# Kernel tuning notes

Measured on AMD Instinct MI355X. Metric: run time of the kernel, lower is better.

Reference implementation:

```python
import jax, jax.numpy as jnp
import numpy as np

BATCH = 32
NUM_PRIORS = 8732
NUM_CLASSES = 81          # includes background class 0
CENTER_VAR = 0.1
SIZE_VAR = 0.2
CONF_THR = 0.01
NMS_THR = 0.45
TOPK = 100                # per-class NMS candidates
MAX_DET = 100             # max detections per image


def setup_inputs() -> dict:
    key = jax.random.key(0)
    k1, k2, k3 = jax.random.split(key, 3)
    cls_logits = jax.random.normal(k1, (BATCH, NUM_PRIORS, NUM_CLASSES), jnp.float32)
    bbox_pred = jax.random.normal(k2, (BATCH, NUM_PRIORS, 4), jnp.float32)
    # center-form priors (cx, cy, w, h) in (0, 1)
    priors = jax.random.uniform(k3, (NUM_PRIORS, 4), jnp.float32, 0.05, 0.95)
    return {"cls_logits": cls_logits, "bbox_pred": bbox_pred, "priors": priors}


def _decode(loc, priors):
    # convert_locations_to_boxes (center form) then center_form_to_corner_form
    cxcy = loc[..., :2] * CENTER_VAR * priors[..., 2:] + priors[..., :2]
    wh = jnp.exp(loc[..., 2:] * SIZE_VAR) * priors[..., 2:]
    return jnp.concatenate([cxcy - wh * 0.5, cxcy + wh * 0.5], axis=-1)  # [.., 4] xyxy


def _pairwise_iou(b):
    # b: [K, 4] corner form
    lt = jnp.maximum(b[:, None, :2], b[None, :, :2])
    rb = jnp.minimum(b[:, None, 2:], b[None, :, 2:])
    wh = jnp.clip(rb - lt, 0.0)
    inter = wh[..., 0] * wh[..., 1]
    area = jnp.clip(b[:, 2] - b[:, 0], 0.0) * jnp.clip(b[:, 3] - b[:, 1], 0.0)
    return inter / (area[:, None] + area[None, :] - inter + 1e-9)


def _per_class_nms(scores_n, boxes_n):
    # scores_n: [N], boxes_n: [N, 4]
    s, idx = jax.lax.top_k(scores_n, TOPK)
    b = boxes_n[idx]                                # [K, 4]
    iou = _pairwise_iou(b)                          # [K, K]
    init = s > CONF_THR
    rng = jnp.arange(TOPK)

    def body(i, keep):
        sup = (iou[i] > NMS_THR) & keep[i] & (rng > i)
        return keep & ~sup

    keep = jax.lax.fori_loop(0, TOPK, body, init)   # greedy NMS on sorted boxes
    return jnp.where(keep, s, 0.0), b


def reference(cls_logits, bbox_pred, priors):
    scores = jax.nn.softmax(cls_logits, axis=-1)            # [B, N, C]
    boxes = _decode(bbox_pred, priors)                      # [B, N, 4]
    cls_scores = jnp.swapaxes(scores[..., 1:], 1, 2)        # [B, C-1, N] skip background
    nms_fn = jax.vmap(jax.vmap(_per_class_nms, in_axes=(0, None)), in_axes=(0, 0))
    s_k, b_k = nms_fn(cls_scores, boxes)                    # [B, C-1, K], [B, C-1, K, 4]
    labels = jnp.broadcast_to(jnp.arange(1, NUM_CLASSES)[None, :, None], s_k.shape)
    B = s_k.shape[0]
    flat = (NUM_CLASSES - 1) * TOPK
    s_f = s_k.reshape(B, flat)
    b_f = b_k.reshape(B, flat, 4)
    l_f = labels.reshape(B, flat)
    top_s, top_i = jax.lax.top_k(s_f, MAX_DET)              # keep best MAX_DET per image
    top_b = jnp.take_along_axis(b_f, top_i[..., None], axis=1)
    top_l = jnp.take_along_axis(l_f, top_i, axis=1)
    return top_b, top_s, top_l.astype(jnp.int32)
```

## Files before the change

kernel.cpp:

```cpp
#include <hip/hip_runtime.h>
#include <hip/hip_bf16.h>
#include <float.h>

#define BATCH    32
#define NPRIORS  8732
#define NT32     274
#define NPAD     (NT32 * 32)
#define NCLASSES 81
#define NC1      80
#define TOPK     100
#define MAXDET   100
#define FLATC    (NC1 * TOPK)
#define FV4      2000
#define NCAND    512
#define NBIN     1024
#define BINOFF   3040
#define NK4      (NT32 * 4)

__global__ __launch_bounds__(256, 4) void softmax_stats_kernel(
    const float* __restrict__ logits, unsigned short* __restrict__ key16,
    float2* __restrict__ stats) {
  int b = blockIdx.x / NT32;
  int tile = blockIdx.x - b * NT32;
  int n0 = tile * 32;
  int rows = min(32, NPRIORS - n0);

  int t = threadIdx.x;
  int r = t >> 3;
  int q = t & 7;

  __shared__ __align__(16) unsigned int ldsu[NC1 * 16];

  const bool live = (r < rows);

  unsigned int out16[10];
  if (live) {
    const float* rowp = logits + ((size_t)b * NPRIORS + n0 + r) * NCLASSES;
    float v[11];
#pragma unroll
    for (int k = 0; k < 10; ++k) v[k] = rowp[q + (k << 3)];
    v[10] = (q == 0) ? rowp[80] : -FLT_MAX;

    float m = -FLT_MAX;
#pragma unroll
    for (int k = 0; k < 10; ++k) m = fmaxf(m, v[k]);
    if (q == 0) m = fmaxf(m, v[10]);
    m = fmaxf(m, __shfl_xor(m, 1));
    m = fmaxf(m, __shfl_xor(m, 2));
    m = fmaxf(m, __shfl_xor(m, 4));

    float s = 0.f;
#pragma unroll
    for (int k = 0; k < 10; ++k) {
      v[k] = expf(v[k] - m);
      s += v[k];
    }
    if (q == 0) {
      v[10] = expf(v[10] - m);
      s += v[10];
    }
    s += __shfl_xor(s, 1);
    s += __shfl_xor(s, 2);
    s += __shfl_xor(s, 4);

#pragma unroll
    for (int k = 0; k < 10; ++k) {
      float sc = v[k] / s;
      out16[k] = __float_as_uint(sc) >> 16;
    }
    if (q == 0) out16[0] = __float_as_uint(v[10] / s) >> 16;
    if (q == 0) stats[(size_t)b * NPAD + n0 + r] = make_float2(m, s);
  } else {
#pragma unroll
    for (int k = 0; k < 10; ++k) out16[k] = 0u;
  }

#pragma unroll
  for (int k = 0; k < 10; ++k) {
    unsigned int part = (unsigned int)__shfl_xor((int)out16[k], 8);
    if ((r & 1) == 0) {
      int cls = (q == 0) ? ((k == 0) ? 79 : (8 * k - 1)) : (q - 1 + 8 * k);
      ldsu[cls * 16 + (r >> 1)] = out16[k] | (part << 16);
    }
  }
  __syncthreads();

  uint4* dst = (uint4*)(key16 + (size_t)(b * NT32 + tile) * (NC1 * 32));
  for (int i = t; i < 320; i += 256) dst[i] = ((const uint4*)ldsu)[i];
}

__device__ __forceinline__ float4 decode_box(float4 l, float4 p) {
  float cx = l.x * 0.1f * p.z + p.x;
  float cy = l.y * 0.1f * p.w + p.y;
  float w  = expf(l.z * 0.2f) * p.z;
  float h  = expf(l.w * 0.2f) * p.w;
  return make_float4(cx - w * 0.5f, cy - h * 0.5f, cx + w * 0.5f,
                     cy + h * 0.5f);
}

__device__ __forceinline__ unsigned long long cex(unsigned long long key,
                                                  unsigned long long p,
                                                  bool up, bool low) {
  return (up == low) ? (key < p ? key : p) : (key > p ? key : p);
}

__global__ __launch_bounds__(256, 8) void topk_select_kernel(
    const unsigned short* __restrict__ key16,
    const float* __restrict__ logits, const float2* __restrict__ stats,
    unsigned long long* __restrict__ k_sel) {
  const int bc = blockIdx.x;
  const int b = bc / NC1;
  const int c = bc - b * NC1;
  const int t = threadIdx.x;
  const int lane = t & 63;
  const int w = t >> 6;

  __shared__ __align__(16) unsigned int hist[NBIN * 2];
  __shared__ __align__(16) unsigned long long cand[NCAND];
  __shared__ __align__(16) unsigned int cidx[NCAND];
  __shared__ int s_cnt, s_cut, wtot[4];

  const uint4* k4 = (const uint4*)key16;
  const size_t base4 = (size_t)b * (NT32 * NC1 * 4) + (size_t)c * 4;

  uint4 va4[5];
#pragma unroll
  for (int i = 0; i < 5; ++i) {
    int p4 = t + (i << 8);
    uint4 v = make_uint4(0u, 0u, 0u, 0u);
    if (p4 < NK4) v = k4[base4 + (size_t)(p4 >> 2) * (NC1 * 4) + (p4 & 3)];
    va4[i] = v;
  }
#pragma unroll
  for (int i = 0; i < 5; ++i)
    asm volatile("" : "+v"(va4[i].x), "+v"(va4[i].y), "+v"(va4[i].z),
                      "+v"(va4[i].w));

  uint4* h4 = (uint4*)hist;
  const uint4 z4 = make_uint4(0u, 0u, 0u, 0u);
  h4[t] = z4;
  h4[t + 256] = z4;
  if (t == 0) { s_cnt = 0; s_cut = 0; }
  __syncthreads();

#pragma unroll
  for (int i = 0; i < 5; ++i) {
    const unsigned int* cp = (const unsigned int*)&va4[i];
#pragma unroll
    for (int u = 0; u < 4; ++u) {
      unsigned int cc = cp[u];
      unsigned int lo = cc & 0xFFFFu, hi = cc >> 16;
      if (lo) {
        int bin = (int)(lo >> 2) - BINOFF;
        bin = max(0, min(NBIN - 1, bin));
        atomicAdd(&hist[(bin << 1) | (lane & 1)], 1u);
      }
      if (hi) {
        int bin = (int)(hi >> 2) - BINOFF;
        bin = max(0, min(NBIN - 1, bin));
        atomicAdd(&hist[(bin << 1) | (lane & 1)], 1u);
      }
    }
  }
  __syncthreads();

  int h[4];
  int ls;
  {
    uint4 a = h4[2 * t];
    uint4 b2 = h4[2 * t + 1];
    h[0] = (int)(a.x + a.y);
    h[1] = (int)(a.z + a.w);
    h[2] = (int)(b2.x + b2.y);
    h[3] = (int)(b2.z + b2.w);
    ls = h[0] + h[1] + h[2] + h[3];
  }
  int s = ls;
#pragma unroll
  for (int off = 1; off < 64; off <<= 1) {
    int o = __shfl_down(s, off);
    if (lane + off < 64) s += o;
  }
  if (lane == 0) wtot[w] = s;
  __syncthreads();
  int upper = 0;
  for (int w2 = w + 1; w2 < 4; ++w2) upper += wtot[w2];
  int run = (s - ls) + upper;
  int cutbin = -1;
#pragma unroll
  for (int k = 3; k >= 0; --k) {
    if (run < TOPK && run + h[k] >= TOPK) cutbin = (t << 2) + k;
    run += h[k];
  }
  if (cutbin >= 0) s_cut = cutbin;
  __syncthreads();

  const unsigned int cutk = (unsigned int)(s_cut + BINOFF) << 2;

  unsigned long long msk = 0ull;
  int cnt = 0;
#pragma unroll
  for (int i = 0; i < 5; ++i) {
    const unsigned int* cp = (const unsigned int*)&va4[i];
#pragma unroll
    for (int u = 0; u < 4; ++u) {
      unsigned int cc = cp[u];
      if ((cc & 0xFFFFu) >= cutk) { msk |= 1ull << (i * 8 + u * 2); ++cnt; }
      if ((cc >> 16) >= cutk)     { msk |= 1ull << (i * 8 + u * 2 + 1); ++cnt; }
    }
  }
  int inc = cnt;
#pragma unroll
  for (int off = 1; off < 64; off <<= 1) {
    int o = __shfl_up(inc, off);
    if (lane >= off) inc += o;
  }
  int wtotal = __shfl(inc, 63);
  int wbase = 0;
  if (lane == 63) wbase = atomicAdd(&s_cnt, wtotal);
  wbase = __shfl(wbase, 63);
  int pos = wbase + inc - cnt;
#pragma unroll
  for (int i = 0; i < 5; ++i) {
    int p4 = t + (i << 8);
    int bpr = ((p4 >> 2) << 5) + ((p4 & 3) << 3);
#pragma unroll
    for (int j = 0; j < 8; ++j) {
      if ((msk >> (i * 8 + j)) & 1ull) {
        if (pos < NCAND) cidx[pos] = (unsigned int)(bpr + j);
        ++pos;
      }
    }
  }
  __syncthreads();

  const int ncand = min(s_cnt, NCAND);

  unsigned long long key = ~0ull;
  if (t < ncand) {
    int p = (int)cidx[t];
    float l = logits[((size_t)b * NPRIORS + p) * NCLASSES + (c + 1)];
    float2 st = stats[(size_t)b * NPAD + p];
    float sc = expf(l - st.x) / st.y;
    key = (((unsigned long long)(~__float_as_uint(sc))) << 32) |
          (unsigned int)p;
  }

  if (ncand <= 256) {
#pragma unroll
    for (int k2 = 2; k2 <= 256; k2 <<= 1) {
#pragma unroll
      for (int j = 128; j > 0; j >>= 1) {
        if (j >= k2) continue;
        const bool up = ((t & k2) == 0);
        if (j >= 64) {
          cand[t] = key;
          __syncthreads();
          unsigned long long p = cand[t ^ j];
          key = cex(key, p, up, (t & j) == 0);
          __syncthreads();
        } else {
          unsigned long long p = __shfl_xor(key, j);
          key = cex(key, p, up, (lane & j) == 0);
        }
      }
    }
    if (t < TOPK) k_sel[(size_t)bc * TOPK + t] = key;
  } else {
    unsigned long long key2 = ~0ull;
    if (t + 256 < ncand) {
      int p = (int)cidx[t + 256];
      float l = logits[((size_t)b * NPRIORS + p) * NCLASSES + (c + 1)];
      float2 st = stats[(size_t)b * NPAD + p];
      float sc = expf(l - st.x) / st.y;
      key2 = (((unsigned long long)(~__float_as_uint(sc))) << 32) |
             (unsigned int)p;
    }
    cand[t] = key;
    cand[t + 256] = key2;
    __syncthreads();
    int NS = 512;
    for (int k2 = 2; k2 <= NS; k2 <<= 1) {
      for (int j = k2 >> 1; j > 0; j >>= 1) {
        if (j >= 128) {
          __syncthreads();
          for (int p = t; p < NS; p += 256) {
            int ixj = p ^ j;
            if (ixj > p) {
              unsigned long long a = cand[p], c2 = cand[ixj];
              bool up = ((p & k2) == 0);
              if (up ? (a > c2) : (a < c2)) { cand[p] = c2; cand[ixj] = a; }
            }
          }
          __syncthreads();
        } else {
          int base = w << 7;
          if (base < NS) {
#pragma unroll
            for (int half = 0; half < 2; ++half) {
              int p = base + lane + (half << 6);
              int ixj = p ^ j;
              if (ixj > p) {
                unsigned long long a = cand[p], c2 = cand[ixj];
                bool up = ((p & k2) == 0);
                if (up ? (a > c2) : (a < c2)) { cand[p] = c2; cand[ixj] = a; }
              }
            }
          }
        }
      }
    }
    __syncthreads();
    if (t < TOPK) k_sel[(size_t)bc * TOPK + t] = cand[t];
  }
}

__global__ __launch_bounds__(256) void nms_kernel(
    const unsigned long long* __restrict__ k_sel,
    const float* __restrict__ loc, const float* __restrict__ priors,
    float* __restrict__ s_k, float* __restrict__ b_k) {
  const int t = threadIdx.x;
  const int lane = t & 63;
  const int w = t >> 6;
  const int bc = blockIdx.x;
  const int b = bc / NC1;

  __shared__ __align__(16) float4 lbox[TOPK];
  __shared__ float larea[TOPK];
  __shared__ float lscore[TOPK];
  __shared__ unsigned long long pm[4][64][3];
  __shared__ unsigned long long keepw[2];

  if (t < TOPK) {
    unsigned long long key = k_sel[(size_t)bc * TOPK + t];
    float sv = __uint_as_float(~(unsigned int)(key >> 32));
    int idx = (int)(key & 0xFFFFFFFFull);
    if ((unsigned)idx >= NPRIORS) { idx = 0; sv = 0.f; }
    float4 bx = decode_box(((const float4*)loc)[(size_t)b * NPRIORS + idx],
                           ((const float4*)priors)[idx]);
    lbox[t] = bx;
    larea[t] = fmaxf(bx.z - bx.x, 0.f) * fmaxf(bx.w - bx.y, 0.f);
    lscore[t] = sv;
  }
  __syncthreads();

  const bool hasb = (lane + 64) < TOPK;
  float4 ba = lbox[lane];
  float aa = larea[lane];
  float4 bb2 = lbox[hasb ? (lane + 64) : 0];
  float ab = larea[hasb ? (lane + 64) : 0];

  unsigned long long ra0 = 0, ra1 = 0, rb1 = 0;
  int jlo = max(1, w * 25);
  int jhi = min(TOPK, w * 25 + 25);
  for (int j = jlo; j < jhi; ++j) {
    float4 bj = lbox[j];
    float aj = larea[j];
    if (lane < j) {
      float iw = fmaxf(fminf(ba.z, bj.z) - fmaxf(ba.x, bj.x), 0.f);
      float ih = fmaxf(fminf(ba.w, bj.w) - fmaxf(ba.y, bj.y), 0.f);
      float inter = iw * ih;
      float iou = inter / (aa + aj - inter + 1e-9f);
      if (iou > 0.45f) {
        if (j < 64) ra0 |= 1ull << j; else ra1 |= 1ull << (j - 64);
      }
    }
    if (hasb && (lane + 64) < j) {
      float iw = fmaxf(fminf(bb2.z, bj.z) - fmaxf(bb2.x, bj.x), 0.f);
      float ih = fmaxf(fminf(bb2.w, bj.w) - fmaxf(bb2.y, bj.y), 0.f);
      float inter = iw * ih;
      float iou = inter / (ab + aj - inter + 1e-9f);
      if (iou > 0.45f) rb1 |= 1ull << (j - 64);
    }
  }
  pm[w][lane][0] = ra0;
  pm[w][lane][1] = ra1;
  pm[w][lane][2] = rb1;
  __syncthreads();

  if (w == 0) {
    unsigned long long fa0 = pm[0][lane][0] | pm[1][lane][0] |
                             pm[2][lane][0] | pm[3][lane][0];
    unsigned long long fa1 = pm[0][lane][1] | pm[1][lane][1] |
                             pm[2][lane][1] | pm[3][lane][1];
    unsigned long long fb1 = pm[0][lane][2] | pm[1][lane][2] |
                             pm[2][lane][2] | pm[3][lane][2];

    float sva = lscore[lane];
    float svb = hasb ? lscore[lane + 64] : 0.f;
    unsigned long long keep0 = __ballot(sva > 0.01f);
    unsigned long long keep1 = __ballot(hasb && (svb > 0.01f));
    for (int i = 0; i < TOPK; ++i) {
      bool il = i < 64;
      bool kb = il ? ((keep0 >> i) & 1ull) : ((keep1 >> (i - 64)) & 1ull);
      unsigned long long m0 = __shfl(il ? fa0 : 0ull, i & 63);
      unsigned long long m1 = __shfl(il ? fa1 : fb1, i & 63);
      if (kb) { keep0 &= ~m0; keep1 &= ~m1; }
    }
    if (lane == 0) { keepw[0] = keep0; keepw[1] = keep1; }
  }
  __syncthreads();

  if (t < TOPK) {
    bool kp = (t < 64) ? ((keepw[0] >> t) & 1ull)
                       : ((keepw[1] >> (t - 64)) & 1ull);
    s_k[(size_t)bc * TOPK + t] = kp ? lscore[t] : 0.f;
    ((float4*)(b_k + (size_t)bc * TOPK * 4))[t] = lbox[t];
  }
}

__global__ __launch_bounds__(256) void final_topk_kernel(
    const float* __restrict__ s_k, const float* __restrict__ b_k,
    float* __restrict__ out) {
  const int b = blockIdx.x;
  const int t = threadIdx.x;
  const int lane = t & 63;
  const int w = t >> 6;

  __shared__ __align__(16) unsigned int hist[NBIN * 2];
  __shared__ __align__(16) unsigned long long cand[NCAND];
  __shared__ int s_cnt, s_cut, wtot[4];

  const float4* src4 = (const float4*)(s_k + (size_t)b * FLATC);

  float va[32];
#pragma unroll
  for (int i = 0; i < 8; ++i) {
    int p = t + (i << 8);
    float4 v = make_float4(0.f, 0.f, 0.f, 0.f);
    if (p < FV4) v = src4[p];
    va[4 * i + 0] = v.x; va[4 * i + 1] = v.y;
    va[4 * i + 2] = v.z; va[4 * i + 3] = v.w;
  }

  uint4* h4 = (uint4*)hist;
  const uint4 z4 = make_uint4(0u, 0u, 0u, 0u);
  h4[t] = z4;
  h4[t + 256] = z4;
  cand[t] = ~0ull;
  cand[t + 256] = ~0ull;
  if (t == 0) { s_cnt = 0; s_cut = 0; }
  __syncthreads();

#pragma unroll
  for (int j = 0; j < 32; ++j) {
    unsigned int bits = __float_as_uint(va[j]);
    if (bits != 0u) {
      int bin = (int)(bits >> 18) - BINOFF;
      bin = max(0, min(NBIN - 1, bin));
      atomicAdd(&hist[(bin << 1) | (lane & 1)], 1u);
    }
  }
  __syncthreads();

  int h[4];
  int ls;
  {
    uint4 a = h4[2 * t];
    uint4 b2 = h4[2 * t + 1];
    h[0] = (int)(a.x + a.y);
    h[1] = (int)(a.z + a.w);
    h[2] = (int)(b2.x + b2.y);
    h[3] = (int)(b2.z + b2.w);
    ls = h[0] + h[1] + h[2] + h[3];
  }
  int s = ls;
#pragma unroll
  for (int off = 1; off < 64; off <<= 1) {
    int o = __shfl_down(s, off);
    if (lane + off < 64) s += o;
  }
  if (lane == 0) wtot[w] = s;
  __syncthreads();
  int upper = 0;
  for (int w2 = w + 1; w2 < 4; ++w2) upper += wtot[w2];
  int run = (s - ls) + upper;
  int cutbin = -1;
#pragma unroll
  for (int k = 3; k >= 0; --k) {
    if (run < TOPK && run + h[k] >= TOPK) cutbin = (t << 2) + k;
    run += h[k];
  }
  if (cutbin >= 0) s_cut = cutbin;
  __syncthreads();

  const unsigned int cutbits = (unsigned int)(s_cut + BINOFF) << 18;

  unsigned int msk = 0u;
  int cnt = 0;
#pragma unroll
  for (int j = 0; j < 32; ++j) {
    unsigned int bits = __float_as_uint(va[j]);
    if (bits >= cutbits) { msk |= 1u << j; ++cnt; }
  }
  int inc = cnt;
#pragma unroll
  for (int off = 1; off < 64; off <<= 1) {
    int o = __shfl_up(inc, off);
    if (lane >= off) inc += o;
  }
  int wtotal = __shfl(inc, 63);
  int wbase = 0;
  if (lane == 63) wbase = atomicAdd(&s_cnt, wtotal);
  wbase = __shfl(wbase, 63);
  int pos = wbase + inc - cnt;
#pragma unroll
  for (int j = 0; j < 32; ++j) {
    if ((msk >> j) & 1u) {
      if (pos < NCAND) {
        unsigned int bits = __float_as_uint(va[j]);
        int idx = ((t + ((j >> 2) << 8)) << 2) + (j & 3);
        cand[pos] = (((unsigned long long)(~bits)) << 32) | (unsigned int)idx;
      }
      ++pos;
    }
  }
  __syncthreads();

  const int ncand = s_cnt;
  unsigned long long okey;
  if (ncand <= 256) {
    unsigned long long key = cand[t];
#pragma unroll
    for (int k2 = 2; k2 <= 256; k2 <<= 1) {
#pragma unroll
      for (int j = 128; j > 0; j >>= 1) {
        if (j >= k2) continue;
        const bool up = ((t & k2) == 0);
        if (j >= 64) {
          cand[t] = key;
          __syncthreads();
          unsigned long long p = cand[t ^ j];
          key = cex(key, p, up, (t & j) == 0);
          __syncthreads();
        } else {
          unsigned long long p = __shfl_xor(key, j);
          key = cex(key, p, up, (lane & j) == 0);
        }
      }
    }
    okey = key;
  } else {
    int NS = 512;
    for (int k2 = 2; k2 <= NS; k2 <<= 1) {
      for (int j = k2 >> 1; j > 0; j >>= 1) {
        if (j >= 128) {
          __syncthreads();
          for (int p = t; p < NS; p += 256) {
            int ixj = p ^ j;
            if (ixj > p) {
              unsigned long long a = cand[p], c2 = cand[ixj];
              bool up = ((p & k2) == 0);
              if (up ? (a > c2) : (a < c2)) { cand[p] = c2; cand[ixj] = a; }
            }
          }
          __syncthreads();
        } else {
          int base = w << 7;
          if (base < NS) {
#pragma unroll
            for (int half = 0; half < 2; ++half) {
              int p = base + lane + (half << 6);
              int ixj = p ^ j;
              if (ixj > p) {
                unsigned long long a = cand[p], c2 = cand[ixj];
                bool up = ((p & k2) == 0);
                if (up ? (a > c2) : (a < c2)) { cand[p] = c2; cand[ixj] = a; }
              }
            }
          }
        }
      }
    }
    __syncthreads();
    okey = cand[min(t, NCAND - 1)];
  }

  if (t < MAXDET) {
    unsigned long long key = okey;
    unsigned int vb = ~(unsigned int)(key >> 32);
    float sv = __uint_as_float(vb);
    int f = (int)(key & 0xFFFFFFFFull);
    if ((unsigned)f >= FLATC) { f = 0; sv = 0.f; }
    float4 bb = *(const float4*)(b_k + ((size_t)b * FLATC + f) * 4);
    ((float4*)out)[b * MAXDET + t] = bb;
    out[BATCH * MAXDET * 4 + b * MAXDET + t] = sv;
    int cls = f / TOPK + 1;
    out[BATCH * MAXDET * 5 + b * MAXDET + t] = (float)cls;
  }
}

extern "C" void kernel_launch(void* const* d_in, const int* in_sizes, int n_in,
                              void* d_out, int out_size, void* d_ws,
                              size_t ws_size, hipStream_t stream) {
  const float* cls_logits = (const float*)d_in[0];
  const float* bbox_pred  = (const float*)d_in[1];
  const float* priors     = (const float*)d_in[2];
  float* out = (float*)d_out;

  unsigned short* key16 = (unsigned short*)d_ws;
  const size_t key16_bytes = (size_t)BATCH * NT32 * NC1 * 32 * 2;
  float2* stats = (float2*)((char*)d_ws + key16_bytes);
  float* s_k = (float*)((char*)stats + (size_t)BATCH * NPAD * sizeof(float2));
  float* b_k = s_k + (size_t)BATCH * NC1 * TOPK;
  unsigned long long* k_sel =
      (unsigned long long*)(b_k + (size_t)BATCH * NC1 * TOPK * 4);

  softmax_stats_kernel<<<BATCH * NT32, 256, 0, stream>>>(cls_logits, key16,
                                                         stats);
  topk_select_kernel<<<BATCH * NC1, 256, 0, stream>>>(key16, cls_logits,
                                                      stats, k_sel);
  nms_kernel<<<BATCH * NC1, 256, 0, stream>>>(k_sel, bbox_pred, priors,
                                              s_k, b_k);
  final_topk_kernel<<<BATCH, 256, 0, stream>>>(s_k, b_k, out);
}
```

Before: 106.4 us.

## Replace histogram cutoff with sample-sort guided threshold search for top-k selection

Drops the 1024-bin shared-memory histogram with atomics in the per-class top-k select. Each thread's first key is bitonic-sorted across the block to seed a threshold ladder, and the threshold is refined by repeated count passes with wave reductions and bisection until the candidate count falls between TOPK and NCAND. This removes histogram zeroing, the LDS atomics and the prefix scan. In exchange it adds a bitonic sort with many barriers and a data-dependent number of counting iterations, each needing its own barrier.

```diff
diff --git a/kernel.cpp b/kernel.cpp
--- a/kernel.cpp
+++ b/kernel.cpp
@@ -115,10 +115,9 @@
   const int lane = t & 63;
   const int w = t >> 6;
 
-  __shared__ __align__(16) unsigned int hist[NBIN * 2];
   __shared__ __align__(16) unsigned long long cand[NCAND];
   __shared__ __align__(16) unsigned int cidx[NCAND];
-  __shared__ int s_cnt, s_cut, wtot[4];
+  __shared__ int s_cnt, wtot[2][4];
 
   const uint4* k4 = (const uint4*)key16;
   const size_t base4 = (size_t)b * (NT32 * NC1 * 4) + (size_t)c * 4;
@@ -131,82 +130,88 @@
     if (p4 < NK4) v = k4[base4 + (size_t)(p4 >> 2) * (NC1 * 4) + (p4 & 3)];
     va4[i] = v;
   }
-#pragma unroll
-  for (int i = 0; i < 5; ++i)
-    asm volatile("" : "+v"(va4[i].x), "+v"(va4[i].y), "+v"(va4[i].z),
-                      "+v"(va4[i].w));
-
-  uint4* h4 = (uint4*)hist;
-  const uint4 z4 = make_uint4(0u, 0u, 0u, 0u);
-  h4[t] = z4;
-  h4[t + 256] = z4;
-  if (t == 0) { s_cnt = 0; s_cut = 0; }
-  __syncthreads();
-
+  if (t == 0) s_cnt = 0;
+
+  unsigned int u = va4[0].x & 0xFFFFu;
+#pragma unroll
+  for (int k2s = 2; k2s <= 256; k2s <<= 1) {
+#pragma unroll
+    for (int j = 128; j > 0; j >>= 1) {
+      if (j >= k2s) continue;
+      const bool up = ((t & k2s) == 0);
+      if (j >= 64) {
+        cidx[t] = u;
+        __syncthreads();
+        unsigned int p = cidx[t ^ j];
+        const bool low = (t & j) == 0;
+        u = (up == low) ? min(u, p) : max(u, p);
+        __syncthreads();
+      } else {
+        unsigned int p = (unsigned int)__shfl_xor((int)u, j);
+        const bool low = (lane & j) == 0;
+        u = (up == low) ? min(u, p) : max(u, p);
+      }
+    }
+  }
+  cidx[t] = u;
+  __syncthreads();
+
+  unsigned int Tlo = 1u;
+  unsigned int Thi = 0x10000u;
+  int kr = 8;
+  unsigned int T = max(cidx[256 - kr], 1u);
+  bool ladder = true;
+  int C = 0;
+  for (int it = 0; it < 20; ++it) {
+    int cc = 0;
+#pragma unroll
+    for (int i = 0; i < 5; ++i) {
+      const unsigned int* cp = (const unsigned int*)&va4[i];
+#pragma unroll
+      for (int uu = 0; uu < 4; ++uu) {
+        unsigned int x = cp[uu];
+        cc += (int)((x & 0xFFFFu) >= T) + (int)((x >> 16) >= T);
+      }
+    }
+#pragma unroll
+    for (int off = 1; off < 64; off <<= 1) cc += __shfl_xor(cc, off);
+    if (lane == 0) wtot[it & 1][w] = cc;
+    __syncthreads();
+    C = wtot[it & 1][0] + wtot[it & 1][1] + wtot[it & 1][2] + wtot[it & 1][3];
+    if (C >= TOPK && C <= NCAND) break;
+    if (C >= TOPK) Tlo = T; else Thi = T;
+    if (Thi <= Tlo + 1u) { T = Tlo; C = TOPK; break; }
+    unsigned int Tn;
+    if (ladder) {
+      kr = (C > NCAND) ? (kr >> 1) : (kr << 1);
+      if (kr < 1 || kr > 128) {
+        ladder = false;
+        Tn = (Tlo + Thi) >> 1;
+      } else {
+        Tn = max(cidx[256 - kr], 1u);
+        if (Tn <= Tlo || Tn >= Thi) { ladder = false; Tn = (Tlo + Thi) >> 1; }
+      }
+    } else {
+      Tn = (Tlo + Thi) >> 1;
+    }
+    T = Tn;
+  }
+  if (C < TOPK) T = Tlo;
+
+  cand[t] = ~0ull;
+  cand[t + 256] = ~0ull;
+  __syncthreads();
+
+  unsigned long long msk = 0ull;
+  int cnt = 0;
 #pragma unroll
   for (int i = 0; i < 5; ++i) {
     const unsigned int* cp = (const unsigned int*)&va4[i];
 #pragma unroll
-    for (int u = 0; u < 4; ++u) {
-      unsigned int cc = cp[u];
-      unsigned int lo = cc & 0xFFFFu, hi = cc >> 16;
-      if (lo) {
-        int bin = (int)(lo >> 2) - BINOFF;
-        bin = max(0, min(NBIN - 1, bin));
-        atomicAdd(&hist[(bin << 1) | (lane & 1)], 1u);
-      }
-      if (hi) {
-        int bin = (int)(hi >> 2) - BINOFF;
-        bin = max(0, min(NBIN - 1, bin));
-        atomicAdd(&hist[(bin << 1) | (lane & 1)], 1u);
-      }
-    }
-  }
-  __syncthreads();
-
-  int h[4];
-  int ls;
-  {
-    uint4 a = h4[2 * t];
-    uint4 b2 = h4[2 * t + 1];
-    h[0] = (int)(a.x + a.y);
-    h[1] = (int)(a.z + a.w);
-    h[2] = (int)(b2.x + b2.y);
-    h[3] = (int)(b2.z + b2.w);
-    ls = h[0] + h[1] + h[2] + h[3];
-  }
-  int s = ls;
-#pragma unroll
-  for (int off = 1; off < 64; off <<= 1) {
-    int o = __shfl_down(s, off);
-    if (lane + off < 64) s += o;
-  }
-  if (lane == 0) wtot[w] = s;
-  __syncthreads();
-  int upper = 0;
-  for (int w2 = w + 1; w2 < 4; ++w2) upper += wtot[w2];
-  int run = (s - ls) + upper;
-  int cutbin = -1;
-#pragma unroll
-  for (int k = 3; k >= 0; --k) {
-    if (run < TOPK && run + h[k] >= TOPK) cutbin = (t << 2) + k;
-    run += h[k];
-  }
-  if (cutbin >= 0) s_cut = cutbin;
-  __syncthreads();
-
-  const unsigned int cutk = (unsigned int)(s_cut + BINOFF) << 2;
-
-  unsigned long long msk = 0ull;
-  int cnt = 0;
-#pragma unroll
-  for (int i = 0; i < 5; ++i) {
-    const unsigned int* cp = (const unsigned int*)&va4[i];
-#pragma unroll
-    for (int u = 0; u < 4; ++u) {
-      unsigned int cc = cp[u];
-      if ((cc & 0xFFFFu) >= cutk) { msk |= 1ull << (i * 8 + u * 2); ++cnt; }
-      if ((cc >> 16) >= cutk)     { msk |= 1ull << (i * 8 + u * 2 + 1); ++cnt; }
+    for (int uu = 0; uu < 4; ++uu) {
+      unsigned int cc = cp[uu];
+      if ((cc & 0xFFFFu) >= T) { msk |= 1ull << (i * 8 + uu * 2); ++cnt; }
+      if ((cc >> 16) >= T)     { msk |= 1ull << (i * 8 + uu * 2 + 1); ++cnt; }
     }
   }
   int inc = cnt;
```

Measured after the change: 120.8 us. 1.14x slower.
